# Optimization experiments

Measured on AMD Instinct MI355X. Metric: run time of the kernel, lower is better.

The kernel has to match this reference:

```python
import jax, jax.numpy as jnp
import numpy as np

N, D, R, DR, H, L = 6000, 128, 1000, 128, 2, 2
MAXN = 1.0 - 4e-3  # Poincare ball projection boundary (c=1)


def _norm(x):
    return jnp.clip(jnp.linalg.norm(x, axis=-1, keepdims=True), 1e-15)


def proj(x):
    n = _norm(x)
    return jnp.where(n > MAXN, x / n * MAXN, x)


def expmap0(u):
    n = _norm(u)
    return proj(jnp.tanh(n) * u / n)


def logmap0(p):
    n = _norm(p)
    return jnp.arctanh(jnp.minimum(n, 1.0 - 1e-7)) * p / n


def mobius_add(x, y):
    x2 = jnp.sum(x * x, -1, keepdims=True)
    y2 = jnp.sum(y * y, -1, keepdims=True)
    xy = jnp.sum(x * y, -1, keepdims=True)
    num = (1 + 2 * xy + y2) * x + (1 - x2) * y
    den = 1 + 2 * xy + x2 * y2
    return num / jnp.clip(den, 1e-15)


def hgc_layer(x, adj, W, b):
    # HypLinear (mobius matvec + hyperbolic bias), HypAgg (tangent-space SpMM), HypAct (relu)
    mv = proj(expmap0(logmap0(x) @ W.T))
    h = proj(mobius_add(mv, proj(expmap0(b))))
    h = proj(expmap0(adj @ logmap0(h)))
    return proj(expmap0(jax.nn.relu(logmap0(h))))


def gat_layer(x, adj, W, a_src, a_dst):
    h = jnp.einsum('nd,hde->hne', x, W)                 # [H,N,D]
    es = jnp.einsum('hne,he->hn', h, a_src)
    ed = jnp.einsum('hne,he->hn', h, a_dst)
    e = jax.nn.leaky_relu(es[:, :, None] + ed[:, None, :], 0.2)  # [H,N,N]
    att = jax.nn.softmax(jnp.where(adj[None] > 0, e, -1e9), axis=-1)
    out = jnp.einsum('hnm,hme->hne', att, h).mean(0)    # head-average -> [N,D]
    return jax.nn.elu(out)


def mha(x, Wq, Wk, Wv, Wfc, g, b):
    # Transformer-style MHA with residual + LayerNorm; x: [N, Lr, D]
    Nn, Lr, _ = x.shape
    split = lambda y: y.reshape(Nn, Lr, H, D).transpose(0, 2, 1, 3)
    q, k, v = split(x @ Wq), split(x @ Wk), split(x @ Wv)
    attn = jax.nn.softmax(jnp.einsum('nhld,nhmd->nhlm', q, k) / jnp.sqrt(jnp.float32(D)), -1)
    o = jnp.einsum('nhlm,nhmd->nhld', attn, v).transpose(0, 2, 1, 3).reshape(Nn, Lr, H * D)
    o = o @ Wfc + x
    mu = o.mean(-1, keepdims=True)
    var = o.var(-1, keepdims=True)
    return g * (o - mu) / jnp.sqrt(var + 1e-6) + b


def _forward(ent_sr, ent_tg, rel_sr, rel_tg, adj_sr, adj_tg, rel_adj_sr, rel_adj_tg,
             gat_W, gat_a_src, gat_a_dst, Wq, Wk, Wv, Wfc, ln_g, ln_b, hgc_W, hgc_b):
    # Relation Aggregator: sparse mm + rowsum normalization
    def rel_agg(radj, remb):
        return (radj @ remb) / radj.sum(-1, keepdims=True)
    sr_rel = rel_agg(rel_adj_sr, rel_sr)
    tg_rel = rel_agg(rel_adj_tg, rel_tg)

    # Attentive Neighbor Aggregator + multi-range fusion (res=True -> range = L+1)
    def branch(x, adj):
        outs, h = [x], x
        for i in range(L):
            h = gat_layer(h, adj, gat_W[i], gat_a_src[i], gat_a_dst[i])
            h = h / jnp.clip(_norm(h), 1e-12)  # F.normalize(dim=1)
            outs.append(h)
        seq = jnp.stack(outs, axis=1)  # [N, L+1, D]
        return mha(seq, Wq, Wk, Wv, Wfc, ln_g, ln_b).mean(1)
    sr = branch(ent_sr, adj_sr)
    tg = branch(ent_tg, adj_tg)

    # Hyperbolic encoder (proj_tan0 is identity for PoincareBall)
    def encode(x, adj):
        h = expmap0(x)
        for i in range(2):
            h = hgc_layer(h, adj, hgc_W[i], hgc_b[i])
        return logmap0(h)
    hs = ent_sr + encode(ent_sr, adj_sr)
    ht = ent_tg + encode(ent_tg, adj_tg)

    return (jnp.concatenate([sr, sr_rel], -1), jnp.concatenate([tg, tg_rel], -1),
            jnp.concatenate([hs, sr_rel], -1), jnp.concatenate([ht, tg_rel], -1))


def setup_inputs() -> dict:
    key = jax.random.key(0)
    ks = jax.random.split(key, 24)

    def make_adj(k):
        m = jax.random.bernoulli(k, 32.0 / N, (N, N)) | jnp.eye(N, dtype=bool)
        a = m.astype(jnp.float32)
        return a / a.sum(-1, keepdims=True)

    def make_rel_adj(k1, k2):
        m = jax.random.bernoulli(k1, 5.0 / R, (N, R)).astype(jnp.float32)
        idx = jax.random.randint(k2, (N,), 0, R)
        return m.at[jnp.arange(N), idx].set(1.0)  # guarantee positive rowsum

    return {
        'ent_sr': 0.02 * jax.random.normal(ks[0], (N, D)),
        'ent_tg': 0.02 * jax.random.normal(ks[1], (N, D)),
        'rel_sr': 0.02 * jax.random.normal(ks[2], (R, DR)),
        'rel_tg': 0.02 * jax.random.normal(ks[3], (R, DR)),
        'adj_sr': make_adj(ks[4]),
        'adj_tg': make_adj(ks[5]),
        'rel_adj_sr': make_rel_adj(ks[6], ks[7]),
        'rel_adj_tg': make_rel_adj(ks[8], ks[9]),
        'gat_W': 0.1 * jax.random.normal(ks[10], (L, H, D, D)),
        'gat_a_src': 0.1 * jax.random.normal(ks[11], (L, H, D)),
        'gat_a_dst': 0.1 * jax.random.normal(ks[12], (L, H, D)),
        'Wq': 0.05 * jax.random.normal(ks[13], (D, H * D)),
        'Wk': 0.05 * jax.random.normal(ks[14], (D, H * D)),
        'Wv': 0.05 * jax.random.normal(ks[15], (D, H * D)),
        'Wfc': 0.05 * jax.random.normal(ks[16], (H * D, D)),
        'ln_g': jnp.ones((D,)),
        'ln_b': jnp.zeros((D,)),
        'hgc_W': 0.05 * jax.random.normal(ks[17], (2, D, D)),
        'hgc_b': 0.01 * jax.random.normal(ks[18], (2, D)),
    }


def reference(ent_sr, ent_tg, rel_sr, rel_tg, adj_sr, adj_tg, rel_adj_sr, rel_adj_tg,
              gat_W, gat_a_src, gat_a_dst, Wq, Wk, Wv, Wfc, ln_g, ln_b, hgc_W, hgc_b):
    return _forward(ent_sr, ent_tg, rel_sr, rel_tg, adj_sr, adj_tg, rel_adj_sr, rel_adj_tg,
                    gat_W, gat_a_src, gat_a_dst, Wq, Wk, Wv, Wfc, ln_g, ln_b, hgc_W, hgc_b)
```

## Files before the change

### kernel.cpp

```cpp
#include <hip/hip_runtime.h>
#include <hip/hip_bf16.h>
#include <math.h>

#define NN   6000
#define N2   12000
#define DD   128
#define RR   1000
#define CAP  96
#define CAPR 48
#define MAXN_F 0.996f

typedef short  bf16x8 __attribute__((ext_vector_type(8)));
typedef float  f32x4  __attribute__((ext_vector_type(4)));
typedef unsigned u32x4 __attribute__((ext_vector_type(4)));

__device__ int      g_dt[19];
__device__ unsigned g_csri[N2 * CAP];
__device__ int      g_cnt[N2];
__device__ float    g_seq[N2 * 3 * DD];
__device__ unsigned short g_seqb[N2 * 3 * DD];
__device__ unsigned short g_hhb[N2 * 256];
__device__ float    g_es[2][N2];
__device__ float    g_ed[2][N2];
__device__ unsigned short g_qkvb[(size_t)N2 * 3 * 768];
__device__ unsigned short g_ob[(size_t)N2 * 3 * 256];
__device__ float    g_fc[N2 * 3 * DD];
__device__ float    g_t[N2 * DD];
__device__ float    g_t2[N2 * DD];
__device__ unsigned short g_WgatT[2][256 * DD];
__device__ unsigned short g_WqkvT[768 * DD];
__device__ unsigned short g_WfcT[DD * 256];
__device__ float    g_WhgcT[2][DD * DD];

__device__ __forceinline__ float ldin(const void* p, size_t i, int bf) {
    if (bf) return __uint_as_float(((unsigned)((const unsigned short*)p)[i]) << 16);
    return ((const float*)p)[i];
}
__device__ __forceinline__ unsigned short f2b(float f) {
    unsigned u = __float_as_uint(f);
    u += 0x7FFFu + ((u >> 16) & 1u);
    return (unsigned short)(u >> 16);
}
__device__ __forceinline__ float b2f(unsigned short b) {
    return __uint_as_float(((unsigned)b) << 16);
}
__device__ __forceinline__ float adjval(int c) {
    return b2f(f2b(1.0f / (float)c));
}

__device__ __forceinline__ float wsum(float v) {
    #pragma unroll
    for (int o = 32; o > 0; o >>= 1) v += __shfl_xor(v, o, 64);
    return v;
}
__device__ __forceinline__ float wmax(float v) {
    #pragma unroll
    for (int o = 32; o > 0; o >>= 1) v = fmaxf(v, __shfl_xor(v, o, 64));
    return v;
}
__device__ __forceinline__ float b128sum(float v, float* r4) {
    v = wsum(v);
    if ((threadIdx.x & 63) == 0) r4[threadIdx.x >> 6] = v;
    __syncthreads();
    float r = r4[0] + r4[1];
    __syncthreads();
    return r;
}
__device__ __forceinline__ void b128sum2(float v0, float v1, float* r4, float& o0, float& o1) {
    v0 = wsum(v0); v1 = wsum(v1);
    int w = threadIdx.x >> 6;
    if ((threadIdx.x & 63) == 0) { r4[w * 2] = v0; r4[w * 2 + 1] = v1; }
    __syncthreads();
    o0 = r4[0] + r4[2]; o1 = r4[1] + r4[3];
    __syncthreads();
}
__device__ __forceinline__ void b128max2(float v0, float v1, float* r4, float& o0, float& o1) {
    v0 = wmax(v0); v1 = wmax(v1);
    int w = threadIdx.x >> 6;
    if ((threadIdx.x & 63) == 0) { r4[w * 2] = v0; r4[w * 2 + 1] = v1; }
    __syncthreads();
    o0 = fmaxf(r4[0], r4[2]); o1 = fmaxf(r4[1], r4[3]);
    __syncthreads();
}

struct P19 { const void* p[19]; };

__global__ void detect_all(P19 ptrs) {
    const int sizes[19] = {768000,768000,128000,128000,36000000,36000000,6000000,6000000,
                           65536,512,512,32768,32768,32768,32768,128,128,32768,256};
    __shared__ int votes[2];
    if (threadIdx.x == 0) { votes[0] = 0; votes[1] = 0; }
    __syncthreads();
    int slot = blockIdx.x < 19 ? blockIdx.x : 17;
    const unsigned* p = (const unsigned*)ptrs.p[slot];
    int nwords = sizes[slot] / 2;
    if (nwords > 0) {
        int nsamp = nwords < 4096 ? nwords : 4096;
        int stride = nwords / nsamp; if (stride < 1) stride = 1;
        for (int s = threadIdx.x; s < nsamp; s += blockDim.x) {
            unsigned lo = p[(size_t)s * stride] & 0xFFFFu;
            if (lo) {
                unsigned e = (lo >> 7) & 0xFFu;
                if (e >= 100u && e <= 140u) atomicAdd(&votes[1], 1);
                else                        atomicAdd(&votes[0], 1);
            }
        }
    }
    __syncthreads();
    int isbf = (votes[1] > votes[0]) ? 1 : 0;
    if (blockIdx.x < 19) {
        if (threadIdx.x == 0) g_dt[blockIdx.x] = isbf;
    } else {
        for (int i = threadIdx.x; i < 32768; i += blockDim.x) {
            int j = i & 127, d = (i >> 7) & 127, l = i >> 14;
            g_WhgcT[l][j * 128 + d] = ldin(ptrs.p[17], i, isbf);
        }
    }
}

__device__ __forceinline__ void bias_wave(const void* hgc_b, int layer, int lane,
                                          float& y0, float& y1, float& y2) {
    float b0 = ldin(hgc_b, (size_t)layer * DD + lane, g_dt[18]);
    float b1 = ldin(hgc_b, (size_t)layer * DD + 64 + lane, g_dt[18]);
    float ss = wsum(b0 * b0 + b1 * b1);
    float nrm = fmaxf(sqrtf(ss), 1e-15f);
    float t = tanhf(nrm);
    float s = t / nrm;
    float vn = t;
    if (t > MAXN_F) { s *= MAXN_F / t; vn = MAXN_F; }
    y0 = s * b0; y1 = s * b1;
    y2 = vn * vn;
}

__device__ __forceinline__ void hgc_lin_w(const float* uw, int layer, int lane,
                                          float y0, float y1, float y2,
                                          float& o0, float& o1) {
    const float* W = g_WhgcT[layer];
    float mv0 = 0.f, mv1 = 0.f;
    #pragma unroll 16
    for (int j = 0; j < DD; j++) {
        float uj = uw[j];
        mv0 = fmaf(W[j * 128 + lane], uj, mv0);
        mv1 = fmaf(W[j * 128 + 64 + lane], uj, mv1);
    }
    float ss2 = wsum(mv0 * mv0 + mv1 * mv1);
    float nm = fmaxf(sqrtf(ss2), 1e-15f);
    float t2 = tanhf(nm);
    float sc = t2 / nm; float xn = t2;
    if (t2 > MAXN_F) { sc *= MAXN_F / t2; xn = MAXN_F; }
    float x0 = sc * mv0, x1 = sc * mv1;
    float x2 = xn * xn;
    float xy = wsum(x0 * y0 + x1 * y1);
    float a = 1.f + 2.f * xy + y2;
    float den = 1.f + 2.f * xy + x2 * y2;
    den = (fabsf(den) < 1e-15f) ? 1e-15f : den;
    float h0 = (a * x0 + (1.f - x2) * y0) / den;
    float h1 = (a * x1 + (1.f - x2) * y1) / den;
    float s3 = wsum(h0 * h0 + h1 * h1);
    float nn = fmaxf(sqrtf(s3), 1e-15f);
    float f = 1.f;
    if (nn > MAXN_F) { f = MAXN_F / nn; nn = MAXN_F; }
    float lg = atanhf(fminf(nn, 1.f - 1e-7f)) / nn;
    o0 = lg * f * h0; o1 = lg * f * h1;
}

__device__ __forceinline__ void hgc_agg_w(const float* tin, int n, int which, int lane,
                                          unsigned* bas, float& o0, float& o1) {
    int c = min(g_cnt[n], CAP);
    const unsigned* idx = &g_csri[(size_t)n * CAP];
    if (lane < c)      bas[lane]      = (idx[lane]      + (unsigned)(which * NN)) * 128u;
    if (64 + lane < c) bas[64 + lane] = (idx[64 + lane] + (unsigned)(which * NN)) * 128u;
    float a0 = 0.f, a1 = 0.f;
    int j = 0;
    for (; j + 4 <= c; j += 4) {
        unsigned b0 = bas[j], b1 = bas[j + 1], b2 = bas[j + 2], b3 = bas[j + 3];
        float v0 = tin[(size_t)b0 + lane], v1 = tin[(size_t)b1 + lane];
        float v2 = tin[(size_t)b2 + lane], v3 = tin[(size_t)b3 + lane];
        float w0 = tin[(size_t)b0 + 64 + lane], w1 = tin[(size_t)b1 + 64 + lane];
        float w2 = tin[(size_t)b2 + 64 + lane], w3 = tin[(size_t)b3 + 64 + lane];
        a0 += (v0 + v1) + (v2 + v3);
        a1 += (w0 + w1) + (w2 + w3);
    }
    for (; j < c; j++) {
        unsigned bb = bas[j];
        a0 += tin[(size_t)bb + lane];
        a1 += tin[(size_t)bb + 64 + lane];
    }
    float sc = (c > 0) ? adjval(c) : 0.f;
    a0 *= sc; a1 *= sc;
    float ss = wsum(a0 * a0 + a1 * a1);
    float nm = fmaxf(sqrtf(ss), 1e-15f);
    float t = tanhf(nm);
    float s1 = t / nm; float xn = t;
    if (t > MAXN_F) { s1 *= MAXN_F / t; xn = MAXN_F; }
    float lg = atanhf(fminf(xn, 1.f - 1e-7f)) / fmaxf(xn, 1e-15f);
    float u0 = fmaxf(lg * s1 * a0, 0.f), u1 = fmaxf(lg * s1 * a1, 0.f);
    float ss2 = wsum(u0 * u0 + u1 * u1);
    float nm2 = fmaxf(sqrtf(ss2), 1e-15f);
    float t2 = tanhf(nm2);
    float s2 = t2 / nm2; float xn2 = t2;
    if (t2 > MAXN_F) { s2 *= MAXN_F / t2; xn2 = MAXN_F; }
    float lg2 = atanhf(fminf(xn2, 1.f - 1e-7f)) / fmaxf(xn2, 1e-15f);
    o0 = lg2 * s2 * u0; o1 = lg2 * s2 * u1;
}

__global__ __launch_bounds__(256) void front_mega(P19 in, float* __restrict__ out) {
    int b = blockIdx.x;
    int tid = threadIdx.x;
    int w = tid >> 6, lane = tid & 63;
    int phase, pb;
    if (b < 9000) { pb = b / 3; phase = b - pb * 3; }
    else { phase = 3; pb = b - 9000; }

    if (phase == 0) {
        int which = pb >= 1500 ? 1 : 0;
        int row = ((which ? pb - 1500 : pb) << 2) | w;
        const void* A = in.p[4 + which];
        int gn = which * NN + row;
        __shared__ int cnt4[4];
        if (lane == 0) cnt4[w] = 0;
        __syncthreads();
        unsigned* dst = &g_csri[(size_t)gn * CAP];
        if (g_dt[4 + which]) {
            const u32x4* p = (const u32x4*)((const unsigned short*)A + (size_t)row * NN);
            #pragma unroll
            for (int c0 = 0; c0 < 12; c0 += 6) {
                u32x4 v[6];
                #pragma unroll
                for (int u = 0; u < 6; u++) {
                    int idx = (c0 + u) * 64 + lane;
                    if (idx < 750) v[u] = __builtin_nontemporal_load(&p[idx]);
                    else v[u] = (u32x4)(0u);
                }
                #pragma unroll
                for (int u = 0; u < 6; u++) {
                    int idx = (c0 + u) * 64 + lane;
                    #pragma unroll
                    for (int h = 0; h < 4; h++) {
                        unsigned w32 = v[u][h];
                        if (w32) {
                            unsigned lo = w32 & 0xFFFFu, hi = w32 >> 16;
                            if (lo && !(lo & 0x8000u)) {
                                int q = atomicAdd(&cnt4[w], 1);
                                if (q < CAP) dst[q] = (unsigned)(idx * 8 + h * 2);
                            }
                            if (hi && !(hi & 0x8000u)) {
                                int q = atomicAdd(&cnt4[w], 1);
                                if (q < CAP) dst[q] = (unsigned)(idx * 8 + h * 2 + 1);
                            }
                        }
                    }
                }
            }
        } else {
            const f32x4* p = (const f32x4*)((const float*)A + (size_t)row * NN);
            #pragma unroll
            for (int c0 = 0; c0 < 24; c0 += 6) {
                f32x4 v[6];
                #pragma unroll
                for (int u = 0; u < 6; u++) {
                    int idx = (c0 + u) * 64 + lane;
                    if (idx < 1500) v[u] = __builtin_nontemporal_load(&p[idx]);
                    else v[u] = (f32x4)(0.f);
                }
                #pragma unroll
                for (int u = 0; u < 6; u++) {
                    int idx = (c0 + u) * 64 + lane;
                    #pragma unroll
                    for (int h = 0; h < 4; h++) {
                        if (v[u][h] > 0.f) {
                            int q = atomicAdd(&cnt4[w], 1);
                            if (q < CAP) dst[q] = (unsigned)(idx * 4 + h);
                        }
                    }
                }
            }
        }
        __syncthreads();
        if (lane == 0) g_cnt[gn] = min(cnt4[w], CAP);
    } else if (phase == 1) {
        int n = pb * 4 + w;
        int which = n >= NN ? 1 : 0;
        int row = n - which * NN;
        const void* radj = in.p[6 + which];
        const void* rel  = in.p[2 + which];
        const int bfa = g_dt[6 + which], bfr = g_dt[2 + which];
        __shared__ int rl_list[4][CAPR];
        __shared__ int rl_cs[4];
        if (lane == 0) rl_cs[w] = 0;
        if (bfa) {
            const uint4* p = (const uint4*)((const unsigned short*)radj + (size_t)row * RR);
            #pragma unroll
            for (int rep = 0; rep < 2; rep++) {
                int i = rep * 64 + lane;
                if (i < 125) {
                    uint4 w4 = p[i];
                    unsigned ws4[4] = {w4.x, w4.y, w4.z, w4.w};
                    #pragma unroll
                    for (int h = 0; h < 4; h++) {
                        unsigned lo = ws4[h] & 0xFFFFu, hi = ws4[h] >> 16;
                        if (lo && !(lo & 0x8000u)) { int q = atomicAdd(&rl_cs[w], 1); if (q < CAPR) rl_list[w][q] = i * 8 + h * 2; }
                        if (hi && !(hi & 0x8000u)) { int q = atomicAdd(&rl_cs[w], 1); if (q < CAPR) rl_list[w][q] = i * 8 + h * 2 + 1; }
                    }
                }
            }
        } else {
            const float4* p = (const float4*)((const float*)radj + (size_t)row * RR);
            #pragma unroll
            for (int rep = 0; rep < 4; rep++) {
                int i = rep * 64 + lane;
                if (i < 250) {
                    float4 w4 = p[i];
                    float vs[4] = {w4.x, w4.y, w4.z, w4.w};
                    #pragma unroll
                    for (int h = 0; h < 4; h++)
                        if (vs[h] > 0.f) { int q = atomicAdd(&rl_cs[w], 1); if (q < CAPR) rl_list[w][q] = i * 4 + h; }
                }
            }
        }
        int c = min(rl_cs[w], CAPR);
        float a0 = 0.f, a1 = 0.f;
        for (int j = 0; j < c; j++) {
            int li = rl_list[w][j];
            a0 += ldin(rel, (size_t)li * DD + lane, bfr);
            a1 += ldin(rel, (size_t)li * DD + 64 + lane, bfr);
        }
        float r0 = c ? a0 / (float)c : 0.f;
        float r1 = c ? a1 / (float)c : 0.f;
        out[(size_t)n * 256 + 128 + lane] = r0;
        out[(size_t)n * 256 + 192 + lane] = r1;
        out[(size_t)(2 * NN + n) * 256 + 128 + lane] = r0;
        out[(size_t)(2 * NN + n) * 256 + 192 + lane] = r1;
    } else if (phase == 2) {
        int n = pb * 4 + w;
        int which = n >= NN ? 1 : 0;
        int row = n - which * NN;
        __shared__ float us[4][128];
        float y0, y1, y2v;
        bias_wave(in.p[18], 0, lane, y0, y1, y2v);
        float x0 = ldin(in.p[which], (size_t)row * DD + lane, g_dt[which]);
        float x1 = ldin(in.p[which], (size_t)row * DD + 64 + lane, g_dt[which]);
        g_seq[(size_t)n * 384 + lane] = x0;
        g_seq[(size_t)n * 384 + 64 + lane] = x1;
        g_seqb[(size_t)n * 384 + lane] = f2b(x0);
        g_seqb[(size_t)n * 384 + 64 + lane] = f2b(x1);
        float ss = wsum(x0 * x0 + x1 * x1);
        float nrm = fmaxf(sqrtf(ss), 1e-15f);
        float t = tanhf(nrm);
        float scale = t / nrm;
        float hn = t;
        if (t > MAXN_F) { scale *= MAXN_F / t; hn = MAXN_F; }
        float lgx = atanhf(fminf(hn, 1.f - 1e-7f)) / fmaxf(hn, 1e-15f);
        us[w][lane] = lgx * scale * x0;
        us[w][64 + lane] = lgx * scale * x1;
        float o0, o1;
        hgc_lin_w(us[w], 0, lane, y0, y1, y2v, o0, o1);
        g_t[(size_t)n * DD + lane] = o0;
        g_t[(size_t)n * DD + 64 + lane] = o1;
    } else {
        int stride = 128 * 256;
        int base = pb * 256 + tid;
        const int b8 = g_dt[8], b11 = g_dt[11], b12 = g_dt[12], b13 = g_dt[13],
                  b14 = g_dt[14];
        for (int i = base; i < 65536; i += stride) {
            int e = i & 127, d = (i >> 7) & 127, h = (i >> 14) & 1, l = (i >> 15) & 1;
            g_WgatT[l][(h * 128 + e) * DD + d] = f2b(ldin(in.p[8], i, b8));
        }
        for (int i = base; i < 32768; i += stride) {
            int d = i >> 8, e = i & 255;
            g_WqkvT[(size_t)e * DD + d]         = f2b(ldin(in.p[11], i, b11));
            g_WqkvT[(size_t)(256 + e) * DD + d] = f2b(ldin(in.p[12], i, b12));
            g_WqkvT[(size_t)(512 + e) * DD + d] = f2b(ldin(in.p[13], i, b13));
        }
        for (int i = base; i < 32768; i += stride) {
            int e = i >> 7, dd = i & 127;
            g_WfcT[dd * 256 + e] = f2b(ldin(in.p[14], i, b14));
        }
    }
}

__global__ __launch_bounds__(256) void gemm_scores(P19 in, int layer) {
    __shared__ __align__(16) unsigned short As[16 * 128 * 8];
    __shared__ __align__(16) unsigned short Bs[16 * 128 * 8];
    int tid = threadIdx.x;
    int gb = blockIdx.x;
    int bm = (gb >> 1) * 128, bn = (gb & 1) * 128;
    const unsigned short* A = g_seqb + layer * 128;
    const int lda = 384;
    const unsigned short* Bt = g_WgatT[layer];
    const int M = N2;
    int lane = tid & 63, w = tid >> 6;
    int q = lane >> 4, ln = lane & 15;
    f32x4 acc[8][2] = {};
    {
        #pragma unroll
        for (int i = 0; i < 8; i++) {
            int combo = w * 8 + i;
            int c = combo >> 1, half = combo & 1;
            int r = half * 64 + lane;
            int gm = bm + r; if (gm >= M) gm = M - 1;
            *(uint4*)&As[(c * 128 + r) * 8] = *(const uint4*)(A + (size_t)gm * lda + c * 8);
            *(uint4*)&Bs[(c * 128 + r) * 8] = *(const uint4*)(Bt + (size_t)(bn + r) * DD + c * 8);
        }
        __syncthreads();
        #pragma unroll
        for (int s = 0; s < 4; s++) {
            bf16x8 bf0 = *(const bf16x8*)&Bs[((s * 4 + q) * 128 + w * 32 + ln) * 8];
            bf16x8 bf1 = *(const bf16x8*)&Bs[((s * 4 + q) * 128 + w * 32 + 16 + ln) * 8];
            #pragma unroll
            for (int mt = 0; mt < 8; mt++) {
                bf16x8 af = *(const bf16x8*)&As[((s * 4 + q) * 128 + mt * 16 + ln) * 8];
                acc[mt][0] = __builtin_amdgcn_mfma_f32_16x16x32_bf16(af, bf0, acc[mt][0], 0, 0, 0);
                acc[mt][1] = __builtin_amdgcn_mfma_f32_16x16x32_bf16(af, bf1, acc[mt][1], 0, 0, 0);
            }
        }
    }
    #pragma unroll
    for (int mt = 0; mt < 8; mt++) {
        #pragma unroll
        for (int nt = 0; nt < 2; nt++) {
            int gcol = bn + w * 32 + nt * 16 + ln;
            #pragma unroll
            for (int r = 0; r < 4; r++) {
                int grow = bm + mt * 16 + q * 4 + r;
                if (grow < M)
                    g_hhb[(size_t)grow * 256 + gcol] = f2b(acc[mt][nt][r]);
            }
        }
    }
    const int head = bn >> 7;
    const int bfs = g_dt[9], bfd = g_dt[10];
    size_t abase = ((size_t)layer * 2 + head) * DD;
    int c0 = w * 32 + ln, c1 = w * 32 + 16 + ln;
    float a0s = ldin(in.p[9],  abase + c0, bfs), a1s = ldin(in.p[9],  abase + c1, bfs);
    float a0d = ldin(in.p[10], abase + c0, bfd), a1d = ldin(in.p[10], abase + c1, bfd);
    __syncthreads();
    float* pS = (float*)As;
    float* pD = pS + 512;
    #pragma unroll
    for (int mt = 0; mt < 8; mt++) {
        #pragma unroll
        for (int r = 0; r < 4; r++) {
            int row = mt * 16 + q * 4 + r;
            float ps = acc[mt][0][r] * a0s + acc[mt][1][r] * a1s;
            float pd = acc[mt][0][r] * a0d + acc[mt][1][r] * a1d;
            #pragma unroll
            for (int o = 1; o < 16; o <<= 1) {
                ps += __shfl_xor(ps, o, 64);
                pd += __shfl_xor(pd, o, 64);
            }
            if (ln == 0) { pS[w * 128 + row] = ps; pD[w * 128 + row] = pd; }
        }
    }
    __syncthreads();
    if (tid < 128) {
        int grow = bm + tid;
        if (grow < M) {
            g_es[head][grow] = pS[tid] + pS[128 + tid] + pS[256 + tid] + pS[384 + tid];
            g_ed[head][grow] = pD[tid] + pD[128 + tid] + pD[256 + tid] + pD[384 + tid];
        }
    }
}

template<bool OUT_BF16>
__global__ __launch_bounds__(256) void gemm_mfma(const unsigned short* __restrict__ A, int lda,
                                                 const unsigned short* __restrict__ Bt, int ldb,
                                                 void* __restrict__ C, int ldc, int M, int K) {
    __shared__ __align__(16) unsigned short As[16 * 128 * 8];
    __shared__ __align__(16) unsigned short Bs[16 * 128 * 8];
    int bm = blockIdx.y * 128, bn = blockIdx.x * 128;
    int tid = threadIdx.x;
    int lane = tid & 63, w = tid >> 6;
    int q = lane >> 4, ln = lane & 15;
    f32x4 acc[8][2] = {};
    for (int k0 = 0; k0 < K; k0 += 128) {
        if (k0 > 0) __syncthreads();
        #pragma unroll
        for (int i = 0; i < 8; i++) {
            int combo = w * 8 + i;
            int c = combo >> 1, half = combo & 1;
            int r = half * 64 + lane;
            int gm = bm + r; if (gm >= M) gm = M - 1;
            *(uint4*)&As[(c * 128 + r) * 8] =
                *(const uint4*)(A + (size_t)gm * lda + k0 + c * 8);
            *(uint4*)&Bs[(c * 128 + r) * 8] =
                *(const uint4*)(Bt + (size_t)(bn + r) * ldb + k0 + c * 8);
        }
        __syncthreads();
        #pragma unroll
        for (int s = 0; s < 4; s++) {
            bf16x8 bf0 = *(const bf16x8*)&Bs[((s * 4 + q) * 128 + w * 32 + ln) * 8];
            bf16x8 bf1 = *(const bf16x8*)&Bs[((s * 4 + q) * 128 + w * 32 + 16 + ln) * 8];
            #pragma unroll
            for (int mt = 0; mt < 8; mt++) {
                bf16x8 af = *(const bf16x8*)&As[((s * 4 + q) * 128 + mt * 16 + ln) * 8];
                acc[mt][0] = __builtin_amdgcn_mfma_f32_16x16x32_bf16(af, bf0, acc[mt][0], 0, 0, 0);
                acc[mt][1] = __builtin_amdgcn_mfma_f32_16x16x32_bf16(af, bf1, acc[mt][1], 0, 0, 0);
            }
        }
    }
    #pragma unroll
    for (int mt = 0; mt < 8; mt++) {
        #pragma unroll
        for (int nt = 0; nt < 2; nt++) {
            int gcol = bn + w * 32 + nt * 16 + ln;
            #pragma unroll
            for (int r = 0; r < 4; r++) {
                int grow = bm + mt * 16 + q * 4 + r;
                if (grow < M) {
                    if (OUT_BF16)
                        ((unsigned short*)C)[(size_t)grow * ldc + gcol] = f2b(acc[mt][nt][r]);
                    else
                        ((float*)C)[(size_t)grow * ldc + gcol] = acc[mt][nt][r];
                }
            }
        }
    }
}

__global__ void gat_attn(int layer) {
    int n = blockIdx.x, d = threadIdx.x;
    int which = n >= NN ? 1 : 0;
    int c = min(g_cnt[n], CAP);
    __shared__ float w0s[CAP], w1s[CAP];
    __shared__ unsigned bases[CAP];
    __shared__ float r4[4];
    __shared__ float sh[256];
    float es0 = g_es[0][n], es1 = g_es[1][n];
    float e0 = -1e30f, e1 = -1e30f;
    if (d < c) {
        int gI = (int)g_csri[(size_t)n * CAP + d] + which * NN;
        bases[d] = (unsigned)gI * 128u;
        e0 = es0 + g_ed[0][gI]; e0 = e0 > 0.f ? e0 : 0.2f * e0;
        e1 = es1 + g_ed[1][gI]; e1 = e1 > 0.f ? e1 : 0.2f * e1;
    }
    float m0, m1, s0, s1;
    b128max2(e0, e1, r4, m0, m1);
    float w0 = (d < c) ? expf(e0 - m0) : 0.f;
    float w1 = (d < c) ? expf(e1 - m1) : 0.f;
    b128sum2(w0, w1, r4, s0, s1);
    if (d < c) { w0s[d] = w0 / fmaxf(s0, 1e-30f); w1s[d] = w1 / fmaxf(s1, 1e-30f); }
    __syncthreads();
    const unsigned* hh32 = (const unsigned*)g_hhb;
    int head = d >> 6;
    const float* wsrc = head ? w1s : w0s;
    float accLo = 0.f, accHi = 0.f;
    int j = 0;
    for (; j + 4 <= c; j += 4) {
        unsigned v0 = hh32[(size_t)bases[j]     + d];
        unsigned v1 = hh32[(size_t)bases[j + 1] + d];
        unsigned v2 = hh32[(size_t)bases[j + 2] + d];
        unsigned v3 = hh32[(size_t)bases[j + 3] + d];
        float g0 = wsrc[j], g1 = wsrc[j + 1], g2 = wsrc[j + 2], g3 = wsrc[j + 3];
        accLo = fmaf(g0, b2f((unsigned short)(v0 & 0xFFFFu)), accLo);
        accHi = fmaf(g0, b2f((unsigned short)(v0 >> 16)), accHi);
        accLo = fmaf(g1, b2f((unsigned short)(v1 & 0xFFFFu)), accLo);
        accHi = fmaf(g1, b2f((unsigned short)(v1 >> 16)), accHi);
        accLo = fmaf(g2, b2f((unsigned short)(v2 & 0xFFFFu)), accLo);
        accHi = fmaf(g2, b2f((unsigned short)(v2 >> 16)), accHi);
        accLo = fmaf(g3, b2f((unsigned short)(v3 & 0xFFFFu)), accLo);
        accHi = fmaf(g3, b2f((unsigned short)(v3 >> 16)), accHi);
    }
    for (; j < c; j++) {
        unsigned wv = hh32[(size_t)bases[j] + d];
        float wgt = wsrc[j];
        accLo = fmaf(wgt, b2f((unsigned short)(wv & 0xFFFFu)), accLo);
        accHi = fmaf(wgt, b2f((unsigned short)(wv >> 16)), accHi);
    }
    sh[2 * d] = accLo; sh[2 * d + 1] = accHi;
    __syncthreads();
    float o = (c > 0) ? 0.5f * (sh[d] + sh[128 + d]) : 0.f;
    o = o > 0.f ? o : expm1f(o);
    __syncthreads();
    float ss = b128sum(o * o, r4);
    float r = o / fmaxf(sqrtf(ss), 1e-12f);
    g_seq[(size_t)n * 384 + (layer + 1) * 128 + d] = r;
    g_seqb[(size_t)n * 384 + (layer + 1) * 128 + d] = f2b(r);
}

__global__ __launch_bounds__(256) void attn_mid(const void* __restrict__ hgc_b) {
    int tid = threadIdx.x;
    if (blockIdx.x < N2) {
        int n = blockIdx.x;
        __shared__ float qs[3][256], ks[3][256], vs[3][256], os[3][256];
        __shared__ float att[2][3][3];
        const unsigned* src = (const unsigned*)(g_qkvb + (size_t)n * 3 * 768);
        for (int t = tid; t < 1152; t += 256) {
            unsigned wv = src[t];
            int l = t / 384, r = t - l * 384;
            int sec = r >> 7, e2 = (r & 127) * 2;
            float f0 = b2f((unsigned short)(wv & 0xFFFFu));
            float f1 = b2f((unsigned short)(wv >> 16));
            float* dstp = (sec == 0) ? qs[l] : (sec == 1) ? ks[l] : vs[l];
            dstp[e2] = f0; dstp[e2 + 1] = f1;
        }
        __syncthreads();
        if (tid < 144) {
            int g = tid >> 3, sub = tid & 7;
            int h = g / 9, lm = g % 9, l = lm / 3, m = lm % 3;
            int d0 = h * 128 + sub * 16;
            float acc = 0.f;
            #pragma unroll
            for (int k = 0; k < 16; k++) acc += qs[l][d0 + k] * ks[m][d0 + k];
            #pragma unroll
            for (int o = 1; o < 8; o <<= 1) acc += __shfl_xor(acc, o, 8);
            if (sub == 0) att[h][l][m] = acc * 0.08838834764831845f;
        }
        __syncthreads();
        if (tid < 6) {
            int h = tid / 3, l = tid % 3;
            float mx = fmaxf(att[h][l][0], fmaxf(att[h][l][1], att[h][l][2]));
            float e0 = expf(att[h][l][0] - mx), e1 = expf(att[h][l][1] - mx), e2 = expf(att[h][l][2] - mx);
            float s = fmaxf(e0 + e1 + e2, 1e-30f);
            att[h][l][0] = e0 / s; att[h][l][1] = e1 / s; att[h][l][2] = e2 / s;
        }
        __syncthreads();
        for (int t = tid; t < 768; t += 256) {
            int l = t >> 8, e = t & 255, h = e >> 7;
            os[l][e] = att[h][l][0] * vs[0][e] + att[h][l][1] * vs[1][e] + att[h][l][2] * vs[2][e];
        }
        __syncthreads();
        unsigned* dst = (unsigned*)(g_ob + (size_t)n * 3 * 256);
        for (int t = tid; t < 384; t += 256) {
            int l = t / 128, e2 = (t % 128) * 2;
            dst[t] = (unsigned)f2b(os[l][e2]) | ((unsigned)f2b(os[l][e2 + 1]) << 16);
        }
    } else {
        int w = tid >> 6, lane = tid & 63;
        int n = (blockIdx.x - N2) * 4 + w;
        int which = n >= NN ? 1 : 0;
        __shared__ unsigned bas[4][CAP];
        __shared__ float us[4][128];
        float y0, y1, y2v;
        bias_wave(hgc_b, 1, lane, y0, y1, y2v);
        float u0, u1;
        hgc_agg_w(g_t, n, which, lane, bas[w], u0, u1);
        us[w][lane] = u0; us[w][64 + lane] = u1;
        float o0, o1;
        hgc_lin_w(us[w], 1, lane, y0, y1, y2v, o0, o1);
        g_t2[(size_t)n * DD + lane] = o0;
        g_t2[(size_t)n * DD + 64 + lane] = o1;
    }
}

__global__ __launch_bounds__(256) void out_fin(const void* __restrict__ g, const void* __restrict__ b,
                                               const void* __restrict__ e0, const void* __restrict__ e1,
                                               float* __restrict__ out) {
    int tid = threadIdx.x;
    int w = tid >> 6, lane = tid & 63;
    if (blockIdx.x < 3000) {
        int n = blockIdx.x * 4 + w;
        const int bg = g_dt[15], bb = g_dt[16];
        float ool0[3], ool1[3], mu[3], rstd[3];
        #pragma unroll
        for (int l = 0; l < 3; l++) {
            ool0[l] = g_fc[(size_t)(n * 3 + l) * 128 + lane] + g_seq[(size_t)(n * 3 + l) * 128 + lane];
            ool1[l] = g_fc[(size_t)(n * 3 + l) * 128 + 64 + lane] + g_seq[(size_t)(n * 3 + l) * 128 + 64 + lane];
        }
        #pragma unroll
        for (int l = 0; l < 3; l++) {
            float s  = wsum(ool0[l] + ool1[l]);
            float ss = wsum(ool0[l] * ool0[l] + ool1[l] * ool1[l]);
            mu[l] = s / 128.f;
            rstd[l] = rsqrtf(ss / 128.f - mu[l] * mu[l] + 1e-6f);
        }
        float acc0 = 0.f, acc1 = 0.f;
        #pragma unroll
        for (int l = 0; l < 3; l++) {
            acc0 += (ool0[l] - mu[l]) * rstd[l];
            acc1 += (ool1[l] - mu[l]) * rstd[l];
        }
        out[(size_t)n * 256 + lane]      = ldin(g, lane, bg) * (acc0 / 3.f) + ldin(b, lane, bb);
        out[(size_t)n * 256 + 64 + lane] = ldin(g, 64 + lane, bg) * (acc1 / 3.f) + ldin(b, 64 + lane, bb);
    } else {
        int n = (blockIdx.x - 3000) * 4 + w;
        int which = n >= NN ? 1 : 0;
        __shared__ unsigned bas[4][CAP];
        float u0, u1;
        hgc_agg_w(g_t2, n, which, lane, bas[w], u0, u1);
        float ev0 = ldin(which ? e1 : e0, (size_t)(n - which * NN) * DD + lane, g_dt[which]);
        float ev1 = ldin(which ? e1 : e0, (size_t)(n - which * NN) * DD + 64 + lane, g_dt[which]);
        out[(size_t)(2 * NN + n) * 256 + lane]      = ev0 + u0;
        out[(size_t)(2 * NN + n) * 256 + 64 + lane] = ev1 + u1;
    }
}

extern "C" void kernel_launch(void* const* d_in, const int* in_sizes, int n_in,
                              void* d_out, int out_size, void* d_ws, size_t ws_size,
                              hipStream_t stream) {
    const void* ln_g = d_in[15];
    const void* ln_b = d_in[16];
    const void* hgc_b = d_in[18];

    float* out = (float*)d_out;

    unsigned short *p_seqb, *p_qkvb, *p_ob, *p_WqkvT, *p_WfcT;
    float *p_fc;
    hipGetSymbolAddress((void**)&p_seqb,  HIP_SYMBOL(g_seqb));
    hipGetSymbolAddress((void**)&p_qkvb,  HIP_SYMBOL(g_qkvb));
    hipGetSymbolAddress((void**)&p_ob,    HIP_SYMBOL(g_ob));
    hipGetSymbolAddress((void**)&p_WqkvT, HIP_SYMBOL(g_WqkvT));
    hipGetSymbolAddress((void**)&p_WfcT,  HIP_SYMBOL(g_WfcT));
    hipGetSymbolAddress((void**)&p_fc,    HIP_SYMBOL(g_fc));

    P19 ptrs;
    for (int i = 0; i < 19; i++) ptrs.p[i] = d_in[i];
    detect_all<<<20, 1024, 0, stream>>>(ptrs);

    front_mega<<<9128, 256, 0, stream>>>(ptrs, out);

    gemm_scores<<<188, 256, 0, stream>>>(ptrs, 0);
    gat_attn<<<N2, 128, 0, stream>>>(0);
    gemm_scores<<<188, 256, 0, stream>>>(ptrs, 1);
    gat_attn<<<N2, 128, 0, stream>>>(1);

    gemm_mfma<true><<<dim3(6, 282), 256, 0, stream>>>(
        p_seqb, 128, p_WqkvT, DD, p_qkvb, 768, N2 * 3, 128);
    attn_mid<<<N2 + 3000, 256, 0, stream>>>(hgc_b);
    gemm_mfma<false><<<dim3(1, 282), 256, 0, stream>>>(
        p_ob, 256, p_WfcT, 256, p_fc, 128, N2 * 3, 256);
    out_fin<<<6000, 256, 0, stream>>>(ln_g, ln_b, d_in[0], d_in[1], out);
}
```

Before: 625.9 us.

## Map one wavefront per node in GAT attention and MHA mid kernels

Rewrites gat_attn and the MHA section of attn_mid so that each 64-lane wavefront handles one node, with four nodes per 256-thread block. Softmax and norm reductions use wave shuffles instead of block-level shared-memory reductions with __syncthreads. In attn_mid, q/k/v are loaded straight into registers with vectorized bf16 loads instead of being staged through shared memory. This aims to cut barrier and LDS overhead and launch fewer blocks, at the cost of more registers per thread and sequential neighbor loops per wave.

```diff
diff --git a/kernel.cpp b/kernel.cpp
--- a/kernel.cpp
+++ b/kernel.cpp
@@ -57,30 +57,6 @@
     #pragma unroll
     for (int o = 32; o > 0; o >>= 1) v = fmaxf(v, __shfl_xor(v, o, 64));
     return v;
-}
-__device__ __forceinline__ float b128sum(float v, float* r4) {
-    v = wsum(v);
-    if ((threadIdx.x & 63) == 0) r4[threadIdx.x >> 6] = v;
-    __syncthreads();
-    float r = r4[0] + r4[1];
-    __syncthreads();
-    return r;
-}
-__device__ __forceinline__ void b128sum2(float v0, float v1, float* r4, float& o0, float& o1) {
-    v0 = wsum(v0); v1 = wsum(v1);
-    int w = threadIdx.x >> 6;
-    if ((threadIdx.x & 63) == 0) { r4[w * 2] = v0; r4[w * 2 + 1] = v1; }
-    __syncthreads();
-    o0 = r4[0] + r4[2]; o1 = r4[1] + r4[3];
-    __syncthreads();
-}
-__device__ __forceinline__ void b128max2(float v0, float v1, float* r4, float& o0, float& o1) {
-    v0 = wmax(v0); v1 = wmax(v1);
-    int w = threadIdx.x >> 6;
-    if ((threadIdx.x & 63) == 0) { r4[w * 2] = v0; r4[w * 2 + 1] = v1; }
-    __syncthreads();
-    o0 = fmaxf(r4[0], r4[2]); o1 = fmaxf(r4[1], r4[3]);
-    __syncthreads();
 }
 
 struct P19 { const void* p[19]; };
@@ -518,116 +494,116 @@
     }
 }
 
-__global__ void gat_attn(int layer) {
-    int n = blockIdx.x, d = threadIdx.x;
+__global__ __launch_bounds__(256) void gat_attn(int layer) {
+    int tid = threadIdx.x;
+    int w = tid >> 6, lane = tid & 63;
+    int n = blockIdx.x * 4 + w;
     int which = n >= NN ? 1 : 0;
     int c = min(g_cnt[n], CAP);
-    __shared__ float w0s[CAP], w1s[CAP];
-    __shared__ unsigned bases[CAP];
-    __shared__ float r4[4];
-    __shared__ float sh[256];
+    __shared__ unsigned bas[4][CAP];
+    __shared__ float w0s[4][CAP], w1s[4][CAP];
     float es0 = g_es[0][n], es1 = g_es[1][n];
-    float e0 = -1e30f, e1 = -1e30f;
-    if (d < c) {
-        int gI = (int)g_csri[(size_t)n * CAP + d] + which * NN;
-        bases[d] = (unsigned)gI * 128u;
-        e0 = es0 + g_ed[0][gI]; e0 = e0 > 0.f ? e0 : 0.2f * e0;
-        e1 = es1 + g_ed[1][gI]; e1 = e1 > 0.f ? e1 : 0.2f * e1;
-    }
-    float m0, m1, s0, s1;
-    b128max2(e0, e1, r4, m0, m1);
-    float w0 = (d < c) ? expf(e0 - m0) : 0.f;
-    float w1 = (d < c) ? expf(e1 - m1) : 0.f;
-    b128sum2(w0, w1, r4, s0, s1);
-    if (d < c) { w0s[d] = w0 / fmaxf(s0, 1e-30f); w1s[d] = w1 / fmaxf(s1, 1e-30f); }
-    __syncthreads();
+    float e0a = -1e30f, e1a = -1e30f, e0b = -1e30f, e1b = -1e30f;
+    if (lane < c) {
+        int gI = (int)g_csri[(size_t)n * CAP + lane] + which * NN;
+        bas[w][lane] = (unsigned)gI * 128u;
+        e0a = es0 + g_ed[0][gI]; e0a = e0a > 0.f ? e0a : 0.2f * e0a;
+        e1a = es1 + g_ed[1][gI]; e1a = e1a > 0.f ? e1a : 0.2f * e1a;
+    }
+    if (64 + lane < c) {
+        int gI = (int)g_csri[(size_t)n * CAP + 64 + lane] + which * NN;
+        bas[w][64 + lane] = (unsigned)gI * 128u;
+        e0b = es0 + g_ed[0][gI]; e0b = e0b > 0.f ? e0b : 0.2f * e0b;
+        e1b = es1 + g_ed[1][gI]; e1b = e1b > 0.f ? e1b : 0.2f * e1b;
+    }
+    float m0 = wmax(fmaxf(e0a, e0b));
+    float m1 = wmax(fmaxf(e1a, e1b));
+    float x0a = (lane < c) ? expf(e0a - m0) : 0.f;
+    float x1a = (lane < c) ? expf(e1a - m1) : 0.f;
+    float x0b = (64 + lane < c) ? expf(e0b - m0) : 0.f;
+    float x1b = (64 + lane < c) ? expf(e1b - m1) : 0.f;
+    float s0 = wsum(x0a + x0b), s1 = wsum(x1a + x1b);
+    float r0 = 1.f / fmaxf(s0, 1e-30f), r1 = 1.f / fmaxf(s1, 1e-30f);
+    if (lane < c)      { w0s[w][lane] = x0a * r0;      w1s[w][lane] = x1a * r1; }
+    if (64 + lane < c) { w0s[w][64 + lane] = x0b * r0; w1s[w][64 + lane] = x1b * r1; }
     const unsigned* hh32 = (const unsigned*)g_hhb;
-    int head = d >> 6;
-    const float* wsrc = head ? w1s : w0s;
-    float accLo = 0.f, accHi = 0.f;
-    int j = 0;
-    for (; j + 4 <= c; j += 4) {
-        unsigned v0 = hh32[(size_t)bases[j]     + d];
-        unsigned v1 = hh32[(size_t)bases[j + 1] + d];
-        unsigned v2 = hh32[(size_t)bases[j + 2] + d];
-        unsigned v3 = hh32[(size_t)bases[j + 3] + d];
-        float g0 = wsrc[j], g1 = wsrc[j + 1], g2 = wsrc[j + 2], g3 = wsrc[j + 3];
-        accLo = fmaf(g0, b2f((unsigned short)(v0 & 0xFFFFu)), accLo);
-        accHi = fmaf(g0, b2f((unsigned short)(v0 >> 16)), accHi);
-        accLo = fmaf(g1, b2f((unsigned short)(v1 & 0xFFFFu)), accLo);
-        accHi = fmaf(g1, b2f((unsigned short)(v1 >> 16)), accHi);
-        accLo = fmaf(g2, b2f((unsigned short)(v2 & 0xFFFFu)), accLo);
-        accHi = fmaf(g2, b2f((unsigned short)(v2 >> 16)), accHi);
-        accLo = fmaf(g3, b2f((unsigned short)(v3 & 0xFFFFu)), accLo);
-        accHi = fmaf(g3, b2f((unsigned short)(v3 >> 16)), accHi);
-    }
-    for (; j < c; j++) {
-        unsigned wv = hh32[(size_t)bases[j] + d];
-        float wgt = wsrc[j];
-        accLo = fmaf(wgt, b2f((unsigned short)(wv & 0xFFFFu)), accLo);
-        accHi = fmaf(wgt, b2f((unsigned short)(wv >> 16)), accHi);
-    }
-    sh[2 * d] = accLo; sh[2 * d + 1] = accHi;
-    __syncthreads();
-    float o = (c > 0) ? 0.5f * (sh[d] + sh[128 + d]) : 0.f;
-    o = o > 0.f ? o : expm1f(o);
-    __syncthreads();
-    float ss = b128sum(o * o, r4);
-    float r = o / fmaxf(sqrtf(ss), 1e-12f);
-    g_seq[(size_t)n * 384 + (layer + 1) * 128 + d] = r;
-    g_seqb[(size_t)n * 384 + (layer + 1) * 128 + d] = f2b(r);
+    float aLe = 0.f, aLo = 0.f, aHe = 0.f, aHo = 0.f;
+    #pragma unroll 4
+    for (int j = 0; j < c; j++) {
+        unsigned bb = bas[w][j];
+        unsigned vlo = hh32[(size_t)bb + lane];
+        unsigned vhi = hh32[(size_t)bb + 64 + lane];
+        float g0 = w0s[w][j], g1 = w1s[w][j];
+        aLe = fmaf(g0, b2f((unsigned short)(vlo & 0xFFFFu)), aLe);
+        aLo = fmaf(g0, b2f((unsigned short)(vlo >> 16)), aLo);
+        aHe = fmaf(g1, b2f((unsigned short)(vhi & 0xFFFFu)), aHe);
+        aHo = fmaf(g1, b2f((unsigned short)(vhi >> 16)), aHo);
+    }
+    float o0 = (c > 0) ? 0.5f * (aLe + aHe) : 0.f;
+    float o1 = (c > 0) ? 0.5f * (aLo + aHo) : 0.f;
+    o0 = o0 > 0.f ? o0 : expm1f(o0);
+    o1 = o1 > 0.f ? o1 : expm1f(o1);
+    float ss = wsum(o0 * o0 + o1 * o1);
+    float rn = 1.f / fmaxf(sqrtf(ss), 1e-12f);
+    o0 *= rn; o1 *= rn;
+    size_t base = (size_t)n * 384 + (layer + 1) * 128 + 2 * lane;
+    g_seq[base] = o0; g_seq[base + 1] = o1;
+    *(unsigned*)&g_seqb[base] = (unsigned)f2b(o0) | ((unsigned)f2b(o1) << 16);
 }
 
 __global__ __launch_bounds__(256) void attn_mid(const void* __restrict__ hgc_b) {
     int tid = threadIdx.x;
-    if (blockIdx.x < N2) {
-        int n = blockIdx.x;
-        __shared__ float qs[3][256], ks[3][256], vs[3][256], os[3][256];
-        __shared__ float att[2][3][3];
-        const unsigned* src = (const unsigned*)(g_qkvb + (size_t)n * 3 * 768);
-        for (int t = tid; t < 1152; t += 256) {
-            unsigned wv = src[t];
-            int l = t / 384, r = t - l * 384;
-            int sec = r >> 7, e2 = (r & 127) * 2;
-            float f0 = b2f((unsigned short)(wv & 0xFFFFu));
-            float f1 = b2f((unsigned short)(wv >> 16));
-            float* dstp = (sec == 0) ? qs[l] : (sec == 1) ? ks[l] : vs[l];
-            dstp[e2] = f0; dstp[e2 + 1] = f1;
-        }
-        __syncthreads();
-        if (tid < 144) {
-            int g = tid >> 3, sub = tid & 7;
-            int h = g / 9, lm = g % 9, l = lm / 3, m = lm % 3;
-            int d0 = h * 128 + sub * 16;
-            float acc = 0.f;
-            #pragma unroll
-            for (int k = 0; k < 16; k++) acc += qs[l][d0 + k] * ks[m][d0 + k];
-            #pragma unroll
-            for (int o = 1; o < 8; o <<= 1) acc += __shfl_xor(acc, o, 8);
-            if (sub == 0) att[h][l][m] = acc * 0.08838834764831845f;
-        }
-        __syncthreads();
-        if (tid < 6) {
-            int h = tid / 3, l = tid % 3;
-            float mx = fmaxf(att[h][l][0], fmaxf(att[h][l][1], att[h][l][2]));
-            float e0 = expf(att[h][l][0] - mx), e1 = expf(att[h][l][1] - mx), e2 = expf(att[h][l][2] - mx);
-            float s = fmaxf(e0 + e1 + e2, 1e-30f);
-            att[h][l][0] = e0 / s; att[h][l][1] = e1 / s; att[h][l][2] = e2 / s;
-        }
-        __syncthreads();
-        for (int t = tid; t < 768; t += 256) {
-            int l = t >> 8, e = t & 255, h = e >> 7;
-            os[l][e] = att[h][l][0] * vs[0][e] + att[h][l][1] * vs[1][e] + att[h][l][2] * vs[2][e];
-        }
-        __syncthreads();
-        unsigned* dst = (unsigned*)(g_ob + (size_t)n * 3 * 256);
-        for (int t = tid; t < 384; t += 256) {
-            int l = t / 128, e2 = (t % 128) * 2;
-            dst[t] = (unsigned)f2b(os[l][e2]) | ((unsigned)f2b(os[l][e2 + 1]) << 16);
+    int w = tid >> 6, lane = tid & 63;
+    if (blockIdx.x < 3000) {
+        int n = blockIdx.x * 4 + w;
+        int d0 = lane * 4;
+        const unsigned short* row = g_qkvb + (size_t)n * 2304;
+        float qf[3][4], kf[3][4], vf[3][4];
+        #pragma unroll
+        for (int l = 0; l < 3; l++) {
+            uint2 qv = *(const uint2*)(row + l * 768 + d0);
+            uint2 kv = *(const uint2*)(row + l * 768 + 256 + d0);
+            uint2 vv = *(const uint2*)(row + l * 768 + 512 + d0);
+            qf[l][0] = b2f((unsigned short)(qv.x & 0xFFFFu)); qf[l][1] = b2f((unsigned short)(qv.x >> 16));
+            qf[l][2] = b2f((unsigned short)(qv.y & 0xFFFFu)); qf[l][3] = b2f((unsigned short)(qv.y >> 16));
+            kf[l][0] = b2f((unsigned short)(kv.x & 0xFFFFu)); kf[l][1] = b2f((unsigned short)(kv.x >> 16));
+            kf[l][2] = b2f((unsigned short)(kv.y & 0xFFFFu)); kf[l][3] = b2f((unsigned short)(kv.y >> 16));
+            vf[l][0] = b2f((unsigned short)(vv.x & 0xFFFFu)); vf[l][1] = b2f((unsigned short)(vv.x >> 16));
+            vf[l][2] = b2f((unsigned short)(vv.y & 0xFFFFu)); vf[l][3] = b2f((unsigned short)(vv.y >> 16));
+        }
+        float att[3][3];
+        #pragma unroll
+        for (int l = 0; l < 3; l++)
+            #pragma unroll
+            for (int m = 0; m < 3; m++) {
+                float p = 0.f;
+                #pragma unroll
+                for (int i = 0; i < 4; i++) p = fmaf(qf[l][i], kf[m][i], p);
+                #pragma unroll
+                for (int o = 16; o > 0; o >>= 1) p += __shfl_xor(p, o, 64);
+                att[l][m] = p * 0.08838834764831845f;
+            }
+        #pragma unroll
+        for (int l = 0; l < 3; l++) {
+            float mx = fmaxf(att[l][0], fmaxf(att[l][1], att[l][2]));
+            float e0 = expf(att[l][0] - mx), e1 = expf(att[l][1] - mx), e2 = expf(att[l][2] - mx);
+            float s = 1.f / fmaxf(e0 + e1 + e2, 1e-30f);
+            att[l][0] = e0 * s; att[l][1] = e1 * s; att[l][2] = e2 * s;
+        }
+        unsigned short* orow = g_ob + (size_t)n * 768;
+        #pragma unroll
+        for (int l = 0; l < 3; l++) {
+            float o[4];
+            #pragma unroll
+            for (int i = 0; i < 4; i++)
+                o[i] = att[l][0] * vf[0][i] + att[l][1] * vf[1][i] + att[l][2] * vf[2][i];
+            uint2 pk;
+            pk.x = (unsigned)f2b(o[0]) | ((unsigned)f2b(o[1]) << 16);
+            pk.y = (unsigned)f2b(o[2]) | ((unsigned)f2b(o[3]) << 16);
+            *(uint2*)(orow + l * 256 + d0) = pk;
         }
     } else {
-        int w = tid >> 6, lane = tid & 63;
-        int n = (blockIdx.x - N2) * 4 + w;
+        int n = (blockIdx.x - 3000) * 4 + w;
         int which = n >= NN ? 1 : 0;
         __shared__ unsigned bas[4][CAP];
         __shared__ float us[4][128];
@@ -710,13 +686,13 @@
     front_mega<<<9128, 256, 0, stream>>>(ptrs, out);
 
     gemm_scores<<<188, 256, 0, stream>>>(ptrs, 0);
-    gat_attn<<<N2, 128, 0, stream>>>(0);
+    gat_attn<<<3000, 256, 0, stream>>>(0);
     gemm_scores<<<188, 256, 0, stream>>>(ptrs, 1);
-    gat_attn<<<N2, 128, 0, stream>>>(1);
+    gat_attn<<<3000, 256, 0, stream>>>(1);
 
     gemm_mfma<true><<<dim3(6, 282), 256, 0, stream>>>(
         p_seqb, 128, p_WqkvT, DD, p_qkvb, 768, N2 * 3, 128);
-    attn_mid<<<N2 + 3000, 256, 0, stream>>>(hgc_b);
+    attn_mid<<<6000, 256, 0, stream>>>(hgc_b);
     gemm_mfma<false><<<dim3(1, 282), 256, 0, stream>>>(
         p_ob, 256, p_WfcT, 256, p_fc, 128, N2 * 3, 256);
     out_fin<<<6000, 256, 0, stream>>>(ln_g, ln_b, d_in[0], d_in[1], out);
```

Result: faster. 607.9 us (-2.9%).
